# Optimization experiments

Hardware: AMD Instinct MI355X
Metric: run time of the kernel (lower is better)

## Reference

```python
import jax, jax.numpy as jnp
import numpy as np

EPS_MEAN = 1e-10


def setup_inputs() -> dict:
    key = jax.random.key(0)
    ks = jax.random.split(key, 16)
    B, N, F, D = 2, 512, 128, 3
    s = lambda fan_in: 1.0 / np.sqrt(fan_in)
    return {
        "h": jax.random.normal(ks[0], (B, N, F), jnp.float32),
        "coord": jax.random.normal(ks[1], (B, N, D), jnp.float32),
        "mask": jnp.ones((B, N), jnp.float32),
        "edge_w1": jax.random.normal(ks[2], (2 * F + 1, F), jnp.float32) * s(2 * F + 1),
        "edge_b1": jnp.zeros((F,), jnp.float32),
        "edge_w2": jax.random.normal(ks[3], (F, F), jnp.float32) * s(F),
        "edge_b2": jnp.zeros((F,), jnp.float32),
        "node_w1": jax.random.normal(ks[4], (2 * F, F), jnp.float32) * s(2 * F),
        "node_b1": jnp.zeros((F,), jnp.float32),
        "node_w2": jax.random.normal(ks[5], (F, F), jnp.float32) * s(F),
        "node_b2": jnp.zeros((F,), jnp.float32),
        "coord_w1": jax.random.normal(ks[6], (F, F), jnp.float32) * s(F),
        "coord_b1": jnp.zeros((F,), jnp.float32),
        # xavier_uniform with gain=0.001 -> tiny weights
        "coord_w2": jax.random.normal(ks[7], (F, 1), jnp.float32) * 0.001 * s(F),
    }


def reference(h, coord, mask, edge_w1, edge_b1, edge_w2, edge_b2,
              node_w1, node_b1, node_w2, node_b2,
              coord_w1, coord_b1, coord_w2):
    silu = jax.nn.silu
    B, N, F = h.shape
    # mask inputs
    h = h * mask[:, :, None]
    coord = coord * mask[:, :, None]
    mask2d = mask[:, :, None] * mask[:, None, :]            # [B,N,N]

    # coord2radial
    coord_diff = coord[:, :, None] - coord[:, None]          # [B,N,N,3]
    radial = jnp.sum(coord_diff ** 2, axis=-1, keepdims=True)  # [B,N,N,1]
    radial = radial * mask2d[..., None]
    coord_diff = coord_diff * mask2d[..., None]

    # edge model: source[b,i,j]=h[b,j], target[b,i,j]=h[b,i]
    source = jnp.broadcast_to(h[:, None, :, :], (B, N, N, F))
    target = jnp.broadcast_to(h[:, :, None, :], (B, N, N, F))
    edge_in = jnp.concatenate([source, target, radial], axis=-1)  # [B,N,N,2F+1]
    m = silu(edge_in @ edge_w1 + edge_b1)
    m = silu(m @ edge_w2 + edge_b2)                          # [B,N,N,F]
    m = m * mask2d[..., None]

    # coord model
    embed = silu(m @ coord_w1 + coord_b1) @ coord_w2         # [B,N,N,1]
    trans = coord_diff * embed * mask2d[..., None]           # [B,N,N,3]
    denom = jnp.sum(mask2d, axis=2, keepdims=True) + EPS_MEAN  # [B,N,1]
    coord_new = coord + jnp.sum(trans, axis=2) / denom
    coord_new = coord_new * mask[:, :, None]

    # node model
    agg = jnp.sum(m, axis=2)                                 # [B,N,F]
    node_in = jnp.concatenate([h, agg], axis=-1) * mask[:, :, None]
    out = silu(node_in @ node_w1 + node_b1) @ node_w2 + node_b2
    h_new = (h + out) * mask[:, :, None]

    return h_new, coord_new
```

## Files before the change

### kernel.cpp

```cpp
#include <hip/hip_runtime.h>


#define B_ 2
#define N_ 512
#define F_ 128
#define TJ 64
#define MSTRIDE 136

#define CM   (-1.44269504088896340736f)
#define INVC (-0.69314718055994530942f)

typedef __attribute__((ext_vector_type(8))) short short8;
typedef __attribute__((ext_vector_type(4))) float floatx4;
typedef __attribute__((ext_vector_type(2))) float floatx2;

#if defined(__has_builtin)
#if __has_builtin(__builtin_amdgcn_exp2f)
#define EXP2F(x) __builtin_amdgcn_exp2f(x)
#endif
#endif
#ifndef EXP2F
#define EXP2F(x) __expf((x) * 0.69314718055994530942f)
#endif

__device__ __forceinline__ float fsilu(float x) {
    float e = __expf(-x);
    return x * __builtin_amdgcn_rcpf(1.0f + e);
}
__device__ __forceinline__ floatx2 mk2(float a, float b) {
    floatx2 r; r.x = a; r.y = b; return r;
}
__device__ __forceinline__ floatx2 silu2s(floatx2 y) {
    floatx2 e;
    e.x = EXP2F(y.x);
    e.y = EXP2F(y.y);
    floatx2 d = e + 1.0f;
    floatx2 r;
    r.x = __uint_as_float(0x7EF311C3u - __float_as_uint(d.x));
    r.y = __uint_as_float(0x7EF311C3u - __float_as_uint(d.y));
    r = r * (2.0f - d * r);
    r = r * (2.0f - d * r);
    return y * r;
}
__device__ __forceinline__ unsigned cvtpk(float lo, float hi) {
    unsigned r;
    asm("v_cvt_pk_bf16_f32 %0, %1, %2" : "=v"(r) : "v"(lo), "v"(hi));
    return r;
}
__device__ __forceinline__ unsigned pack2(float a, float b) {
    return __builtin_amdgcn_perm(__float_as_uint(b) + 0x8000u,
                                 __float_as_uint(a) + 0x8000u, 0x07060302u);
}

__global__ __launch_bounds__(256) void egcl_prep(
        const float* __restrict__ h, const float* __restrict__ mask,
        const float* __restrict__ ew1, const float* __restrict__ ew2,
        const float* __restrict__ cw1,
        float* __restrict__ Hs, float* __restrict__ Ht,
        unsigned short* __restrict__ W2P, unsigned short* __restrict__ WcP,
        float* __restrict__ msum) {
    __shared__ float sh[8][F_];
    const int blk = blockIdx.x, tid = threadIdx.x;
    if (blk < 128) {
        const int r0 = blk * 8;
        const int col = tid & 127, half = tid >> 7;
#pragma unroll
        for (int rr = 0; rr < 4; ++rr) {
            int row = rr * 2 + half;
            sh[row][col] = h[(r0 + row) * F_ + col] * mask[r0 + row];
        }
        __syncthreads();
        const float* W = ew1 + half * F_ * F_ + col;
        float acc[8] = {0.f, 0.f, 0.f, 0.f, 0.f, 0.f, 0.f, 0.f};
#pragma unroll 8
        for (int k = 0; k < F_; ++k) {
            float w = W[k * F_];
#pragma unroll
            for (int r = 0; r < 8; ++r) acc[r] += sh[r][k] * w;
        }
        float* dst = half ? Ht : Hs;
#pragma unroll
        for (int r = 0; r < 8; ++r) dst[(r0 + r) * F_ + col] = acc[r] * CM;
    } else if (blk < 144) {
        const int wsel = (blk - 128) >> 3;
        const int mt = (blk - 128) & 7;
        const float* src = wsel ? cw1 : ew2;
        unsigned short* dst = wsel ? WcP : W2P;
        const int ln = tid & 63, kk = tid >> 6;
        const int qq = ln >> 4, ll = ln & 15;
#pragma unroll
        for (int rep = 0; rep < 2; ++rep) {
            const int krow = kk * 32 + qq * 8 + rep * 4;
            float f0 = src[(krow + 0) * F_ + mt * 16 + ll];
            float f1 = src[(krow + 1) * F_ + mt * 16 + ll];
            float f2 = src[(krow + 2) * F_ + mt * 16 + ll];
            float f3 = src[(krow + 3) * F_ + mt * 16 + ll];
            uint2 u = make_uint2(pack2(f0, f1), pack2(f2, f3));
            *(uint2*)(dst + ((mt * 4 + kk) * 64 + ln) * 8 + rep * 4) = u;
        }
    } else {
        const int bb = blk - 144;
        float v = mask[bb * N_ + tid] + mask[bb * N_ + 256 + tid];
        v += __shfl_xor(v, 1);  v += __shfl_xor(v, 2);
        v += __shfl_xor(v, 4);  v += __shfl_xor(v, 8);
        v += __shfl_xor(v, 16); v += __shfl_xor(v, 32);
        const int wave = tid >> 6, lane = tid & 63;
        if (lane == 0) sh[0][wave] = v;
        __syncthreads();
        if (tid == 0) msum[bb] = sh[0][0] + sh[0][1] + sh[0][2] + sh[0][3];
    }
}

#define L_M1   0
#define L_M    17408
#define L_HB   34816
#define L_W1R  35328
#define L_EMBP 35840
#define L_HIN  36864
#define L_RAD  37376
#define L_F2   37632
#define L_TOTAL 37888
#define L_AGG  0
#define L_AGGT 512
#define L_TL   1024
#define L_NP   1536
#define L_CSW  2560

__global__ __launch_bounds__(256, 2) void egcl_main(
        const float* __restrict__ h, const float* __restrict__ coord,
        const float* __restrict__ mask,
        const float* __restrict__ eb1, const float* __restrict__ eb2,
        const float* __restrict__ cb1, const float* __restrict__ cw2,
        const float* __restrict__ nw1, const float* __restrict__ nb1,
        const float* __restrict__ nw2, const float* __restrict__ nb2,
        const float* __restrict__ ew1,
        const float* __restrict__ Hs, const float* __restrict__ Ht,
        const unsigned short* __restrict__ W2P,
        const unsigned short* __restrict__ WcP,
        const float* __restrict__ msum,
        float* __restrict__ out_h, float* __restrict__ out_coord) {
    extern __shared__ char smem[];
    unsigned short* m1s = (unsigned short*)(smem + L_M1);
    unsigned short* ms  = (unsigned short*)(smem + L_M);
    float* HB    = (float*)(smem + L_HB);
    float* W1R   = (float*)(smem + L_W1R);
    float* embp  = (float*)(smem + L_EMBP);
    float* hin   = (float*)(smem + L_HIN);
    float* radl  = (float*)(smem + L_RAD);
    float* f2l   = (float*)(smem + L_F2);
    float* aggs  = (float*)(smem + L_AGG);
    float* aggt  = (float*)(smem + L_AGGT);
    float* tl    = (float*)(smem + L_TL);
    float* np    = (float*)(smem + L_NP);
    float* csw   = (float*)(smem + L_CSW);

    const int tid  = threadIdx.x;
    const int wave = tid >> 6, lane = tid & 63;
    const int q = lane >> 4, l15 = lane & 15;
    const int wg = wave;
    const int bi = blockIdx.x;
    const int b  = bi >> 9;
    const float mask_i = mask[bi];

    short8 w2f[2][4], wcf[2][4];
#pragma unroll
    for (int s = 0; s < 2; ++s)
#pragma unroll
        for (int kk = 0; kk < 4; ++kk) {
            w2f[s][kk] = *(const short8*)(W2P + (((2 * wg + s) * 4 + kk) * 64 + lane) * 8);
            wcf[s][kk] = *(const short8*)(WcP + (((2 * wg + s) * 4 + kk) * 64 + lane) * 8);
        }
    floatx4 e2b[2], c1b[2];
    floatx2 w2c2[4];
#pragma unroll
    for (int s = 0; s < 2; ++s) {
        e2b[s] = (*(const floatx4*)(eb2 + wg * 32 + s * 16 + q * 4)) * CM;
        c1b[s] = (*(const floatx4*)(cb1 + wg * 32 + s * 16 + q * 4)) * CM;
    }
    {
        floatx4 w0 = *(const floatx4*)(cw2 + wg * 32 + 0 * 16 + q * 4);
        floatx4 w1 = *(const floatx4*)(cw2 + wg * 32 + 1 * 16 + q * 4);
        w2c2[0] = mk2(w0[0], w0[1]) * INVC;
        w2c2[1] = mk2(w0[2], w0[3]) * INVC;
        w2c2[2] = mk2(w1[0], w1[1]) * INVC;
        w2c2[3] = mk2(w1[2], w1[3]) * INVC;
    }

    if (tid < F_) {
        HB[tid]  = Ht[bi * F_ + tid] + CM * eb1[tid];
        W1R[tid] = CM * ew1[2 * F_ * F_ + tid];
        hin[tid] = h[bi * F_ + tid] * mask_i;
    }
    const float cmi0 = coord[bi * 3 + 0] * mask_i;
    const float cmi1 = coord[bi * 3 + 1] * mask_i;
    const float cmi2 = coord[bi * 3 + 2] * mask_i;
    if (tid < TJ) {
        int jg = b * N_ + tid;
        float mj = mask[jg];
        float c0 = coord[jg * 3 + 0] * mj;
        float c1 = coord[jg * 3 + 1] * mj;
        float c2 = coord[jg * 3 + 2] * mj;
        float d0 = cmi0 - c0, d1 = cmi1 - c1, d2 = cmi2 - c2;
        float ff = mask_i * mj;
        radl[tid] = (d0 * d0 + d1 * d1 + d2 * d2) * ff;
        f2l[tid]  = ff;
    }
    __syncthreads();

    const int kseg = tid & 15, jq = tid >> 4;
    floatx2 hbk2[4], w1k2[4];
    {
        const floatx4* hp = (const floatx4*)(HB + kseg * 8);
        const floatx4* wp = (const floatx4*)(W1R + kseg * 8);
        floatx4 a = hp[0], bb2 = hp[1], cc = wp[0], dd = wp[1];
        hbk2[0] = mk2(a[0], a[1]);   hbk2[1] = mk2(a[2], a[3]);
        hbk2[2] = mk2(bb2[0], bb2[1]); hbk2[3] = mk2(bb2[2], bb2[3]);
        w1k2[0] = mk2(cc[0], cc[1]); w1k2[1] = mk2(cc[2], cc[3]);
        w1k2[2] = mk2(dd[0], dd[1]); w1k2[3] = mk2(dd[2], dd[3]);
    }
    floatx2 ag[4];
    ag[0] = mk2(0.f, 0.f); ag[1] = mk2(0.f, 0.f);
    ag[2] = mk2(0.f, 0.f); ag[3] = mk2(0.f, 0.f);
    float cs0 = 0.f, cs1 = 0.f, cs2 = 0.f;

    for (int p = 0; p < N_ / TJ; ++p) {
#pragma unroll
        for (int r = 0; r < 4; ++r) {
            int row = jq * 4 + r;
            int jg = b * N_ + p * TJ + row;
            float radm = radl[row];
            floatx2 rr = mk2(radm, radm);
            const floatx4* hsp = (const floatx4*)(Hs + jg * F_ + kseg * 8);
            floatx4 h0 = hsp[0], h1 = hsp[1];
            floatx2 y0 = mk2(h0[0], h0[1]) + hbk2[0] + rr * w1k2[0];
            floatx2 y1 = mk2(h0[2], h0[3]) + hbk2[1] + rr * w1k2[1];
            floatx2 y2 = mk2(h1[0], h1[1]) + hbk2[2] + rr * w1k2[2];
            floatx2 y3 = mk2(h1[2], h1[3]) + hbk2[3] + rr * w1k2[3];
            floatx2 x0 = silu2s(y0), x1 = silu2s(y1);
            floatx2 x2 = silu2s(y2), x3 = silu2s(y3);
            union { short8 s8; unsigned u[4]; } pu;
            pu.u[0] = cvtpk(x0.x, x0.y); pu.u[1] = cvtpk(x1.x, x1.y);
            pu.u[2] = cvtpk(x2.x, x2.y); pu.u[3] = cvtpk(x3.x, x3.y);
            *(short8*)(m1s + row * MSTRIDE + kseg * 8) = pu.s8;
        }
        __syncthreads();
#pragma unroll
        for (int jt = 0; jt < 4; ++jt) {
            const int jrow = jt * 16 + l15;
            const unsigned short* m1r = m1s + jrow * MSTRIDE;
            floatx4 a0 = e2b[0], a1 = e2b[1];
#pragma unroll
            for (int kk = 0; kk < 4; ++kk) {
                short8 bf = *(const short8*)(m1r + kk * 32 + q * 8);
                a0 = __builtin_amdgcn_mfma_f32_16x16x32_bf16(w2f[0][kk], bf, a0, 0, 0, 0);
                a1 = __builtin_amdgcn_mfma_f32_16x16x32_bf16(w2f[1][kk], bf, a1, 0, 0, 0);
            }
            const float f2 = f2l[jrow];
            floatx2 f22 = mk2(f2, f2);
            floatx2 p0 = silu2s(mk2(a0[0], a0[1])) * f22;
            floatx2 p1 = silu2s(mk2(a0[2], a0[3])) * f22;
            floatx2 p2 = silu2s(mk2(a1[0], a1[1])) * f22;
            floatx2 p3 = silu2s(mk2(a1[2], a1[3])) * f22;
            ag[0] += p0; ag[1] += p1; ag[2] += p2; ag[3] += p3;
            unsigned short* mr = ms + jrow * MSTRIDE + wg * 32 + q * 4;
            *(uint2*)(mr)      = make_uint2(cvtpk(p0.x, p0.y), cvtpk(p1.x, p1.y));
            *(uint2*)(mr + 16) = make_uint2(cvtpk(p2.x, p2.y), cvtpk(p3.x, p3.y));
        }
        __syncthreads();
#pragma unroll
        for (int jt = 0; jt < 4; ++jt) {
            const int jrow = jt * 16 + l15;
            const unsigned short* mr = ms + jrow * MSTRIDE;
            floatx4 a0 = c1b[0], a1 = c1b[1];
#pragma unroll
            for (int kk = 0; kk < 4; ++kk) {
                short8 bf = *(const short8*)(mr + kk * 32 + q * 8);
                a0 = __builtin_amdgcn_mfma_f32_16x16x32_bf16(wcf[0][kk], bf, a0, 0, 0, 0);
                a1 = __builtin_amdgcn_mfma_f32_16x16x32_bf16(wcf[1][kk], bf, a1, 0, 0, 0);
            }
            floatx2 esv = mk2(0.f, 0.f);
            esv += silu2s(mk2(a0[0], a0[1])) * w2c2[0];
            esv += silu2s(mk2(a0[2], a0[3])) * w2c2[1];
            esv += silu2s(mk2(a1[0], a1[1])) * w2c2[2];
            esv += silu2s(mk2(a1[2], a1[3])) * w2c2[3];
            float es = esv.x + esv.y;
            es += __shfl_xor(es, 16);
            es += __shfl_xor(es, 32);
            if (q == 0) embp[wg * 64 + jrow] = es;
        }
        if (p < N_ / TJ - 1 && wave == 1) {
            int jg = b * N_ + (p + 1) * TJ + lane;
            float mj = mask[jg];
            float c0 = coord[jg * 3 + 0] * mj;
            float c1 = coord[jg * 3 + 1] * mj;
            float c2 = coord[jg * 3 + 2] * mj;
            float d0 = cmi0 - c0, d1 = cmi1 - c1, d2 = cmi2 - c2;
            float ff = mask_i * mj;
            radl[lane] = (d0 * d0 + d1 * d1 + d2 * d2) * ff;
            f2l[lane]  = ff;
        }
        __syncthreads();
        if (tid < TJ) {
            float e = embp[tid] + embp[64 + tid] + embp[128 + tid] + embp[192 + tid];
            int jg = b * N_ + p * TJ + tid;
            float mj = mask[jg];
            float c0 = coord[jg * 3 + 0] * mj;
            float c1 = coord[jg * 3 + 1] * mj;
            float c2 = coord[jg * 3 + 2] * mj;
            float f2 = mask_i * mj;
            float w = e * f2 * f2;
            cs0 += (cmi0 - c0) * w;
            cs1 += (cmi1 - c1) * w;
            cs2 += (cmi2 - c2) * w;
        }
    }

    float agf[8] = {ag[0].x, ag[0].y, ag[1].x, ag[1].y,
                    ag[2].x, ag[2].y, ag[3].x, ag[3].y};
#pragma unroll
    for (int rg = 0; rg < 8; ++rg) {
        float v = agf[rg];
        v += __shfl_xor(v, 1); v += __shfl_xor(v, 2);
        v += __shfl_xor(v, 4); v += __shfl_xor(v, 8);
        agf[rg] = v;
    }
    if (l15 == 0) {
        floatx4 o0 = {agf[0], agf[1], agf[2], agf[3]};
        floatx4 o1 = {agf[4], agf[5], agf[6], agf[7]};
        *(floatx4*)(aggs + wg * 32 + q * 4)      = o0;
        *(floatx4*)(aggs + wg * 32 + 16 + q * 4) = o1;
    }
    if (wave == 0) {
        cs0 += __shfl_xor(cs0, 1); cs0 += __shfl_xor(cs0, 2);
        cs0 += __shfl_xor(cs0, 4); cs0 += __shfl_xor(cs0, 8);
        cs0 += __shfl_xor(cs0, 16); cs0 += __shfl_xor(cs0, 32);
        cs1 += __shfl_xor(cs1, 1); cs1 += __shfl_xor(cs1, 2);
        cs1 += __shfl_xor(cs1, 4); cs1 += __shfl_xor(cs1, 8);
        cs1 += __shfl_xor(cs1, 16); cs1 += __shfl_xor(cs1, 32);
        cs2 += __shfl_xor(cs2, 1); cs2 += __shfl_xor(cs2, 2);
        cs2 += __shfl_xor(cs2, 4); cs2 += __shfl_xor(cs2, 8);
        cs2 += __shfl_xor(cs2, 16); cs2 += __shfl_xor(cs2, 32);
        if (lane == 0) {
            csw[0] = cs0; csw[1] = cs1; csw[2] = cs2;
        }
    }
    __syncthreads();
    if (tid < F_) aggt[tid] = aggs[tid] * (mask_i * INVC);
    __syncthreads();
    {
        int half = tid >> 7, col = tid & 127;
        const float* W = nw1 + half * 128 * F_ + col;
        float s = 0.f;
        if (half == 0) {
#pragma unroll 8
            for (int k = 0; k < F_; ++k) s += hin[k] * W[k * F_];
            s *= mask_i;
        } else {
#pragma unroll 8
            for (int k = 0; k < F_; ++k) s += aggt[k] * W[k * F_];
        }
        np[tid] = s;
    }
    __syncthreads();
    if (tid < F_) tl[tid] = fsilu(np[tid] + np[128 + tid] + nb1[tid]);
    __syncthreads();
    if (tid < F_) {
        float s = nb2[tid];
#pragma unroll 8
        for (int k = 0; k < F_; ++k) s += tl[k] * nw2[k * F_ + tid];
        out_h[bi * F_ + tid] = (hin[tid] + s) * mask_i;
    } else if (tid < F_ + 3) {
        int d = tid - F_;
        float denom = mask_i * msum[b] + 1e-10f;
        float cm = (d == 0) ? cmi0 : ((d == 1) ? cmi1 : cmi2);
        out_coord[bi * 3 + d] = (cm + csw[d] * __builtin_amdgcn_rcpf(denom)) * mask_i;
    }
}

extern "C" void kernel_launch(void* const* d_in, const int* in_sizes, int n_in,
                              void* d_out, int out_size, void* d_ws, size_t ws_size,
                              hipStream_t stream) {
    const float* h     = (const float*)d_in[0];
    const float* coord = (const float*)d_in[1];
    const float* mask  = (const float*)d_in[2];
    const float* ew1   = (const float*)d_in[3];
    const float* eb1   = (const float*)d_in[4];
    const float* ew2   = (const float*)d_in[5];
    const float* eb2   = (const float*)d_in[6];
    const float* nw1   = (const float*)d_in[7];
    const float* nb1   = (const float*)d_in[8];
    const float* nw2   = (const float*)d_in[9];
    const float* nb2   = (const float*)d_in[10];
    const float* cw1   = (const float*)d_in[11];
    const float* cb1   = (const float*)d_in[12];
    const float* cw2   = (const float*)d_in[13];

    float* Hs = (float*)d_ws;
    float* Ht = Hs + B_ * N_ * F_;
    unsigned short* W2P = (unsigned short*)(Ht + B_ * N_ * F_);
    unsigned short* WcP = W2P + F_ * F_;
    float* msum = (float*)(WcP + F_ * F_);

    float* out_h = (float*)d_out;
    float* out_coord = out_h + B_ * N_ * F_;

    egcl_prep<<<146, 256, 0, stream>>>(h, mask, ew1, ew2, cw1,
                                       Hs, Ht, W2P, WcP, msum);
    egcl_main<<<B_ * N_, 256, L_TOTAL, stream>>>(
        h, coord, mask, eb1, eb2, cb1, cw2, nw1, nb1, nw2, nb2, ew1,
        Hs, Ht, W2P, WcP, msum, out_h, out_coord);
}
```

Measured before the change: 177.5 us.

## Restructure edge loop: per-wave row ownership with register layer-1 fragments and LDS weights

The block grows to 512 threads, and each wave owns 32 neighbour rows per pass, with the j-tile enlarged to 256. The first edge layer is computed straight into MFMA B-fragments in registers instead of being staged through shared memory. The per-iteration block barriers and cross-wave embedding reduction are removed: edge and coord weights are copied once per block into a large LDS region, and each wave reduces its own coordinate partials. In exchange, LDS use rises to about 138KB per block, which limits occupancy. Every block also re-copies 64KB of packed weights from global memory, and weight fragments are re-read from LDS on every MFMA step instead of sitting in registers.

```diff
diff --git a/kernel.cpp b/kernel.cpp
--- a/kernel.cpp
+++ b/kernel.cpp
@@ -4,7 +4,7 @@
 #define B_ 2
 #define N_ 512
 #define F_ 128
-#define TJ 64
+#define TJ 256
 #define MSTRIDE 136
 
 #define CM   (-1.44269504088896340736f)
@@ -111,22 +111,23 @@
     }
 }
 
-#define L_M1   0
-#define L_M    17408
-#define L_HB   34816
-#define L_W1R  35328
-#define L_EMBP 35840
-#define L_HIN  36864
-#define L_RAD  37376
-#define L_F2   37632
-#define L_TOTAL 37888
-#define L_AGG  0
-#define L_AGGT 512
-#define L_TL   1024
-#define L_NP   1536
-#define L_CSW  2560
-
-__global__ __launch_bounds__(256, 2) void egcl_main(
+#define L_W2   0
+#define L_WC   32768
+#define L_MS   65536
+#define L_HB   135168
+#define L_W1R  135680
+#define L_EB2  136192
+#define L_CB1  136704
+#define L_CW2  137216
+#define L_HIN  137728
+#define L_TOTAL 138240
+#define L_AGGP (L_MS + 0)
+#define L_CSP  (L_MS + 4096)
+#define L_NP   (L_MS + 4224)
+#define L_TL   (L_MS + 6272)
+#define L_AGGT (L_MS + 6784)
+
+__global__ __launch_bounds__(512, 2) void egcl_main(
         const float* __restrict__ h, const float* __restrict__ coord,
         const float* __restrict__ mask,
         const float* __restrict__ eb1, const float* __restrict__ eb2,
@@ -140,229 +141,229 @@
         const float* __restrict__ msum,
         float* __restrict__ out_h, float* __restrict__ out_coord) {
     extern __shared__ char smem[];
-    unsigned short* m1s = (unsigned short*)(smem + L_M1);
-    unsigned short* ms  = (unsigned short*)(smem + L_M);
+    unsigned short* W2L = (unsigned short*)(smem + L_W2);
+    unsigned short* WcL = (unsigned short*)(smem + L_WC);
+    unsigned short* ms  = (unsigned short*)(smem + L_MS);
     float* HB    = (float*)(smem + L_HB);
     float* W1R   = (float*)(smem + L_W1R);
-    float* embp  = (float*)(smem + L_EMBP);
+    float* EB2s  = (float*)(smem + L_EB2);
+    float* CB1s  = (float*)(smem + L_CB1);
+    float* CW2s  = (float*)(smem + L_CW2);
     float* hin   = (float*)(smem + L_HIN);
-    float* radl  = (float*)(smem + L_RAD);
-    float* f2l   = (float*)(smem + L_F2);
-    float* aggs  = (float*)(smem + L_AGG);
+    float* aggp  = (float*)(smem + L_AGGP);
+    float* csp   = (float*)(smem + L_CSP);
+    float* np    = (float*)(smem + L_NP);
+    float* tl    = (float*)(smem + L_TL);
     float* aggt  = (float*)(smem + L_AGGT);
-    float* tl    = (float*)(smem + L_TL);
-    float* np    = (float*)(smem + L_NP);
-    float* csw   = (float*)(smem + L_CSW);
 
     const int tid  = threadIdx.x;
     const int wave = tid >> 6, lane = tid & 63;
     const int q = lane >> 4, l15 = lane & 15;
-    const int wg = wave;
     const int bi = blockIdx.x;
     const int b  = bi >> 9;
     const float mask_i = mask[bi];
 
-    short8 w2f[2][4], wcf[2][4];
-#pragma unroll
-    for (int s = 0; s < 2; ++s)
-#pragma unroll
-        for (int kk = 0; kk < 4; ++kk) {
-            w2f[s][kk] = *(const short8*)(W2P + (((2 * wg + s) * 4 + kk) * 64 + lane) * 8);
-            wcf[s][kk] = *(const short8*)(WcP + (((2 * wg + s) * 4 + kk) * 64 + lane) * 8);
-        }
-    floatx4 e2b[2], c1b[2];
-    floatx2 w2c2[4];
-#pragma unroll
-    for (int s = 0; s < 2; ++s) {
-        e2b[s] = (*(const floatx4*)(eb2 + wg * 32 + s * 16 + q * 4)) * CM;
-        c1b[s] = (*(const floatx4*)(cb1 + wg * 32 + s * 16 + q * 4)) * CM;
-    }
     {
-        floatx4 w0 = *(const floatx4*)(cw2 + wg * 32 + 0 * 16 + q * 4);
-        floatx4 w1 = *(const floatx4*)(cw2 + wg * 32 + 1 * 16 + q * 4);
-        w2c2[0] = mk2(w0[0], w0[1]) * INVC;
-        w2c2[1] = mk2(w0[2], w0[3]) * INVC;
-        w2c2[2] = mk2(w1[0], w1[1]) * INVC;
-        w2c2[3] = mk2(w1[2], w1[3]) * INVC;
-    }
-
+        const uint4* s2 = (const uint4*)W2P;
+        const uint4* sc = (const uint4*)WcP;
+        uint4* d2 = (uint4*)(smem + L_W2);
+        uint4* dc = (uint4*)(smem + L_WC);
+#pragma unroll
+        for (int t = 0; t < 4; ++t) {
+            d2[tid + t * 512] = s2[tid + t * 512];
+            dc[tid + t * 512] = sc[tid + t * 512];
+        }
+    }
     if (tid < F_) {
-        HB[tid]  = Ht[bi * F_ + tid] + CM * eb1[tid];
-        W1R[tid] = CM * ew1[2 * F_ * F_ + tid];
-        hin[tid] = h[bi * F_ + tid] * mask_i;
+        HB[tid]   = Ht[bi * F_ + tid] + CM * eb1[tid];
+        W1R[tid]  = CM * ew1[2 * F_ * F_ + tid];
+        EB2s[tid] = CM * eb2[tid];
+        CB1s[tid] = CM * cb1[tid];
+        CW2s[tid] = INVC * cw2[tid];
+        hin[tid]  = h[bi * F_ + tid] * mask_i;
     }
     const float cmi0 = coord[bi * 3 + 0] * mask_i;
     const float cmi1 = coord[bi * 3 + 1] * mask_i;
     const float cmi2 = coord[bi * 3 + 2] * mask_i;
-    if (tid < TJ) {
-        int jg = b * N_ + tid;
-        float mj = mask[jg];
-        float c0 = coord[jg * 3 + 0] * mj;
-        float c1 = coord[jg * 3 + 1] * mj;
-        float c2 = coord[jg * 3 + 2] * mj;
-        float d0 = cmi0 - c0, d1 = cmi1 - c1, d2 = cmi2 - c2;
-        float ff = mask_i * mj;
-        radl[tid] = (d0 * d0 + d1 * d1 + d2 * d2) * ff;
-        f2l[tid]  = ff;
-    }
-    __syncthreads();
-
-    const int kseg = tid & 15, jq = tid >> 4;
-    floatx2 hbk2[4], w1k2[4];
+    __syncthreads();
+
+    const int j0 = wave * 32 + l15;
+    const int j1 = j0 + 16;
+    unsigned short* msr0 = ms + j0 * MSTRIDE;
+    unsigned short* msr1 = ms + j1 * MSTRIDE;
+
+    floatx2 ag2[16];
+#pragma unroll
+    for (int t = 0; t < 16; ++t) ag2[t] = mk2(0.f, 0.f);
+    float cs0 = 0.f, cs1 = 0.f, cs2 = 0.f;
+
+    for (int p = 0; p < N_ / TJ; ++p) {
+        const int jg0 = b * N_ + p * TJ + j0;
+        const int jg1 = jg0 + 16;
+        const float mj0 = mask[jg0], mj1 = mask[jg1];
+        const float c00 = coord[jg0 * 3 + 0] * mj0;
+        const float c01 = coord[jg0 * 3 + 1] * mj0;
+        const float c02 = coord[jg0 * 3 + 2] * mj0;
+        const float c10 = coord[jg1 * 3 + 0] * mj1;
+        const float c11 = coord[jg1 * 3 + 1] * mj1;
+        const float c12 = coord[jg1 * 3 + 2] * mj1;
+        const float d00 = cmi0 - c00, d01 = cmi1 - c01, d02 = cmi2 - c02;
+        const float d10 = cmi0 - c10, d11 = cmi1 - c11, d12 = cmi2 - c12;
+        const float f2_0 = mask_i * mj0, f2_1 = mask_i * mj1;
+        const float rad0 = (d00 * d00 + d01 * d01 + d02 * d02) * f2_0;
+        const float rad1 = (d10 * d10 + d11 * d11 + d12 * d12) * f2_1;
+        const floatx2 rr0 = mk2(rad0, rad0), rr1 = mk2(rad1, rad1);
+        const floatx2 f220 = mk2(f2_0, f2_0), f221 = mk2(f2_1, f2_1);
+
+        short8 bfr0[4], bfr1[4];
+#pragma unroll
+        for (int kk = 0; kk < 4; ++kk) {
+            const int ko = kk * 32 + q * 8;
+            floatx4 hb0 = *(const floatx4*)(HB + ko);
+            floatx4 hb1 = *(const floatx4*)(HB + ko + 4);
+            floatx4 w10 = *(const floatx4*)(W1R + ko);
+            floatx4 w11 = *(const floatx4*)(W1R + ko + 4);
+            {
+                floatx4 hsA = *(const floatx4*)(Hs + jg0 * F_ + ko);
+                floatx4 hsB = *(const floatx4*)(Hs + jg0 * F_ + ko + 4);
+                floatx2 y0 = mk2(hsA[0], hsA[1]) + mk2(hb0[0], hb0[1]) + rr0 * mk2(w10[0], w10[1]);
+                floatx2 y1 = mk2(hsA[2], hsA[3]) + mk2(hb0[2], hb0[3]) + rr0 * mk2(w10[2], w10[3]);
+                floatx2 y2 = mk2(hsB[0], hsB[1]) + mk2(hb1[0], hb1[1]) + rr0 * mk2(w11[0], w11[1]);
+                floatx2 y3 = mk2(hsB[2], hsB[3]) + mk2(hb1[2], hb1[3]) + rr0 * mk2(w11[2], w11[3]);
+                floatx2 x0 = silu2s(y0), x1 = silu2s(y1);
+                floatx2 x2 = silu2s(y2), x3 = silu2s(y3);
+                union { short8 s8; unsigned u[4]; } pu;
+                pu.u[0] = cvtpk(x0.x, x0.y); pu.u[1] = cvtpk(x1.x, x1.y);
+                pu.u[2] = cvtpk(x2.x, x2.y); pu.u[3] = cvtpk(x3.x, x3.y);
+                bfr0[kk] = pu.s8;
+            }
+            {
+                floatx4 hsA = *(const floatx4*)(Hs + jg1 * F_ + ko);
+                floatx4 hsB = *(const floatx4*)(Hs + jg1 * F_ + ko + 4);
+                floatx2 y0 = mk2(hsA[0], hsA[1]) + mk2(hb0[0], hb0[1]) + rr1 * mk2(w10[0], w10[1]);
+                floatx2 y1 = mk2(hsA[2], hsA[3]) + mk2(hb0[2], hb0[3]) + rr1 * mk2(w10[2], w10[3]);
+                floatx2 y2 = mk2(hsB[0], hsB[1]) + mk2(hb1[0], hb1[1]) + rr1 * mk2(w11[0], w11[1]);
+                floatx2 y3 = mk2(hsB[2], hsB[3]) + mk2(hb1[2], hb1[3]) + rr1 * mk2(w11[2], w11[3]);
+                floatx2 x0 = silu2s(y0), x1 = silu2s(y1);
+                floatx2 x2 = silu2s(y2), x3 = silu2s(y3);
+                union { short8 s8; unsigned u[4]; } pu;
+                pu.u[0] = cvtpk(x0.x, x0.y); pu.u[1] = cvtpk(x1.x, x1.y);
+                pu.u[2] = cvtpk(x2.x, x2.y); pu.u[3] = cvtpk(x3.x, x3.y);
+                bfr1[kk] = pu.s8;
+            }
+        }
+
+#pragma unroll
+        for (int s = 0; s < 8; ++s) {
+            floatx4 bias = *(const floatx4*)(EB2s + s * 16 + q * 4);
+            floatx4 a0 = bias, a1 = bias;
+#pragma unroll
+            for (int kk = 0; kk < 4; ++kk) {
+                short8 wf = *(const short8*)(W2L + ((s * 4 + kk) * 64 + lane) * 8);
+                a0 = __builtin_amdgcn_mfma_f32_16x16x32_bf16(wf, bfr0[kk], a0, 0, 0, 0);
+                a1 = __builtin_amdgcn_mfma_f32_16x16x32_bf16(wf, bfr1[kk], a1, 0, 0, 0);
+            }
+            floatx2 p00 = silu2s(mk2(a0[0], a0[1])) * f220;
+            floatx2 p01 = silu2s(mk2(a0[2], a0[3])) * f220;
+            floatx2 p10 = silu2s(mk2(a1[0], a1[1])) * f221;
+            floatx2 p11 = silu2s(mk2(a1[2], a1[3])) * f221;
+            ag2[2 * s]     += p00 + p10;
+            ag2[2 * s + 1] += p01 + p11;
+            *(uint2*)(msr0 + s * 16 + q * 4) =
+                make_uint2(cvtpk(p00.x, p00.y), cvtpk(p01.x, p01.y));
+            *(uint2*)(msr1 + s * 16 + q * 4) =
+                make_uint2(cvtpk(p10.x, p10.y), cvtpk(p11.x, p11.y));
+        }
+
+        short8 mfr0[4], mfr1[4];
+#pragma unroll
+        for (int kk = 0; kk < 4; ++kk) {
+            mfr0[kk] = *(const short8*)(msr0 + kk * 32 + q * 8);
+            mfr1[kk] = *(const short8*)(msr1 + kk * 32 + q * 8);
+        }
+        floatx2 esv0 = mk2(0.f, 0.f), esv1 = mk2(0.f, 0.f);
+#pragma unroll
+        for (int s = 0; s < 8; ++s) {
+            floatx4 cb = *(const floatx4*)(CB1s + s * 16 + q * 4);
+            floatx4 a0 = cb, a1 = cb;
+#pragma unroll
+            for (int kk = 0; kk < 4; ++kk) {
+                short8 wf = *(const short8*)(WcL + ((s * 4 + kk) * 64 + lane) * 8);
+                a0 = __builtin_amdgcn_mfma_f32_16x16x32_bf16(wf, mfr0[kk], a0, 0, 0, 0);
+                a1 = __builtin_amdgcn_mfma_f32_16x16x32_bf16(wf, mfr1[kk], a1, 0, 0, 0);
+            }
+            floatx4 wv = *(const floatx4*)(CW2s + s * 16 + q * 4);
+            esv0 += silu2s(mk2(a0[0], a0[1])) * mk2(wv[0], wv[1]);
+            esv0 += silu2s(mk2(a0[2], a0[3])) * mk2(wv[2], wv[3]);
+            esv1 += silu2s(mk2(a1[0], a1[1])) * mk2(wv[0], wv[1]);
+            esv1 += silu2s(mk2(a1[2], a1[3])) * mk2(wv[2], wv[3]);
+        }
+        float es0 = esv0.x + esv0.y;
+        float es1 = esv1.x + esv1.y;
+        es0 += __shfl_xor(es0, 16); es0 += __shfl_xor(es0, 32);
+        es1 += __shfl_xor(es1, 16); es1 += __shfl_xor(es1, 32);
+        if (q == 0) {
+            float w0 = es0 * f2_0 * f2_0;
+            float w1 = es1 * f2_1 * f2_1;
+            cs0 += d00 * w0 + d10 * w1;
+            cs1 += d01 * w0 + d11 * w1;
+            cs2 += d02 * w0 + d12 * w1;
+        }
+    }
+
+#pragma unroll
+    for (int t = 0; t < 16; ++t) {
+        float vx = ag2[t].x, vy = ag2[t].y;
+        vx += __shfl_xor(vx, 1); vx += __shfl_xor(vx, 2);
+        vx += __shfl_xor(vx, 4); vx += __shfl_xor(vx, 8);
+        vy += __shfl_xor(vy, 1); vy += __shfl_xor(vy, 2);
+        vy += __shfl_xor(vy, 4); vy += __shfl_xor(vy, 8);
+        ag2[t] = mk2(vx, vy);
+    }
+    cs0 += __shfl_xor(cs0, 1); cs0 += __shfl_xor(cs0, 2);
+    cs0 += __shfl_xor(cs0, 4); cs0 += __shfl_xor(cs0, 8);
+    cs1 += __shfl_xor(cs1, 1); cs1 += __shfl_xor(cs1, 2);
+    cs1 += __shfl_xor(cs1, 4); cs1 += __shfl_xor(cs1, 8);
+    cs2 += __shfl_xor(cs2, 1); cs2 += __shfl_xor(cs2, 2);
+    cs2 += __shfl_xor(cs2, 4); cs2 += __shfl_xor(cs2, 8);
+
+    __syncthreads();
+    if (l15 == 0) {
+#pragma unroll
+        for (int s = 0; s < 8; ++s) {
+            floatx4 o = {ag2[2 * s].x, ag2[2 * s].y,
+                         ag2[2 * s + 1].x, ag2[2 * s + 1].y};
+            *(floatx4*)(aggp + wave * F_ + s * 16 + q * 4) = o;
+        }
+    }
+    if (lane == 0) {
+        csp[wave * 3 + 0] = cs0;
+        csp[wave * 3 + 1] = cs1;
+        csp[wave * 3 + 2] = cs2;
+    }
+    __syncthreads();
+    if (tid < F_) {
+        float s = 0.f;
+#pragma unroll
+        for (int w = 0; w < 8; ++w) s += aggp[w * F_ + tid];
+        aggt[tid] = s * (mask_i * INVC);
+    }
+    __syncthreads();
     {
-        const floatx4* hp = (const floatx4*)(HB + kseg * 8);
-        const floatx4* wp = (const floatx4*)(W1R + kseg * 8);
-        floatx4 a = hp[0], bb2 = hp[1], cc = wp[0], dd = wp[1];
-        hbk2[0] = mk2(a[0], a[1]);   hbk2[1] = mk2(a[2], a[3]);
-        hbk2[2] = mk2(bb2[0], bb2[1]); hbk2[3] = mk2(bb2[2], bb2[3]);
-        w1k2[0] = mk2(cc[0], cc[1]); w1k2[1] = mk2(cc[2], cc[3]);
-        w1k2[2] = mk2(dd[0], dd[1]); w1k2[3] = mk2(dd[2], dd[3]);
-    }
-    floatx2 ag[4];
-    ag[0] = mk2(0.f, 0.f); ag[1] = mk2(0.f, 0.f);
-    ag[2] = mk2(0.f, 0.f); ag[3] = mk2(0.f, 0.f);
-    float cs0 = 0.f, cs1 = 0.f, cs2 = 0.f;
-
-    for (int p = 0; p < N_ / TJ; ++p) {
-#pragma unroll
-        for (int r = 0; r < 4; ++r) {
-            int row = jq * 4 + r;
-            int jg = b * N_ + p * TJ + row;
-            float radm = radl[row];
-            floatx2 rr = mk2(radm, radm);
-            const floatx4* hsp = (const floatx4*)(Hs + jg * F_ + kseg * 8);
-            floatx4 h0 = hsp[0], h1 = hsp[1];
-            floatx2 y0 = mk2(h0[0], h0[1]) + hbk2[0] + rr * w1k2[0];
-            floatx2 y1 = mk2(h0[2], h0[3]) + hbk2[1] + rr * w1k2[1];
-            floatx2 y2 = mk2(h1[0], h1[1]) + hbk2[2] + rr * w1k2[2];
-            floatx2 y3 = mk2(h1[2], h1[3]) + hbk2[3] + rr * w1k2[3];
-            floatx2 x0 = silu2s(y0), x1 = silu2s(y1);
-            floatx2 x2 = silu2s(y2), x3 = silu2s(y3);
-            union { short8 s8; unsigned u[4]; } pu;
-            pu.u[0] = cvtpk(x0.x, x0.y); pu.u[1] = cvtpk(x1.x, x1.y);
-            pu.u[2] = cvtpk(x2.x, x2.y); pu.u[3] = cvtpk(x3.x, x3.y);
-            *(short8*)(m1s + row * MSTRIDE + kseg * 8) = pu.s8;
-        }
-        __syncthreads();
-#pragma unroll
-        for (int jt = 0; jt < 4; ++jt) {
-            const int jrow = jt * 16 + l15;
-            const unsigned short* m1r = m1s + jrow * MSTRIDE;
-            floatx4 a0 = e2b[0], a1 = e2b[1];
-#pragma unroll
-            for (int kk = 0; kk < 4; ++kk) {
-                short8 bf = *(const short8*)(m1r + kk * 32 + q * 8);
-                a0 = __builtin_amdgcn_mfma_f32_16x16x32_bf16(w2f[0][kk], bf, a0, 0, 0, 0);
-                a1 = __builtin_amdgcn_mfma_f32_16x16x32_bf16(w2f[1][kk], bf, a1, 0, 0, 0);
-            }
-            const float f2 = f2l[jrow];
-            floatx2 f22 = mk2(f2, f2);
-            floatx2 p0 = silu2s(mk2(a0[0], a0[1])) * f22;
-            floatx2 p1 = silu2s(mk2(a0[2], a0[3])) * f22;
-            floatx2 p2 = silu2s(mk2(a1[0], a1[1])) * f22;
-            floatx2 p3 = silu2s(mk2(a1[2], a1[3])) * f22;
-            ag[0] += p0; ag[1] += p1; ag[2] += p2; ag[3] += p3;
-            unsigned short* mr = ms + jrow * MSTRIDE + wg * 32 + q * 4;
-            *(uint2*)(mr)      = make_uint2(cvtpk(p0.x, p0.y), cvtpk(p1.x, p1.y));
-            *(uint2*)(mr + 16) = make_uint2(cvtpk(p2.x, p2.y), cvtpk(p3.x, p3.y));
-        }
-        __syncthreads();
-#pragma unroll
-        for (int jt = 0; jt < 4; ++jt) {
-            const int jrow = jt * 16 + l15;
-            const unsigned short* mr = ms + jrow * MSTRIDE;
-            floatx4 a0 = c1b[0], a1 = c1b[1];
-#pragma unroll
-            for (int kk = 0; kk < 4; ++kk) {
-                short8 bf = *(const short8*)(mr + kk * 32 + q * 8);
-                a0 = __builtin_amdgcn_mfma_f32_16x16x32_bf16(wcf[0][kk], bf, a0, 0, 0, 0);
-                a1 = __builtin_amdgcn_mfma_f32_16x16x32_bf16(wcf[1][kk], bf, a1, 0, 0, 0);
-            }
-            floatx2 esv = mk2(0.f, 0.f);
-            esv += silu2s(mk2(a0[0], a0[1])) * w2c2[0];
-            esv += silu2s(mk2(a0[2], a0[3])) * w2c2[1];
-            esv += silu2s(mk2(a1[0], a1[1])) * w2c2[2];
-            esv += silu2s(mk2(a1[2], a1[3])) * w2c2[3];
-            float es = esv.x + esv.y;
-            es += __shfl_xor(es, 16);
-            es += __shfl_xor(es, 32);
-            if (q == 0) embp[wg * 64 + jrow] = es;
-        }
-        if (p < N_ / TJ - 1 && wave == 1) {
-            int jg = b * N_ + (p + 1) * TJ + lane;
-            float mj = mask[jg];
-            float c0 = coord[jg * 3 + 0] * mj;
-            float c1 = coord[jg * 3 + 1] * mj;
-            float c2 = coord[jg * 3 + 2] * mj;
-            float d0 = cmi0 - c0, d1 = cmi1 - c1, d2 = cmi2 - c2;
-            float ff = mask_i * mj;
-            radl[lane] = (d0 * d0 + d1 * d1 + d2 * d2) * ff;
-            f2l[lane]  = ff;
-        }
-        __syncthreads();
-        if (tid < TJ) {
-            float e = embp[tid] + embp[64 + tid] + embp[128 + tid] + embp[192 + tid];
-            int jg = b * N_ + p * TJ + tid;
-            float mj = mask[jg];
-            float c0 = coord[jg * 3 + 0] * mj;
-            float c1 = coord[jg * 3 + 1] * mj;
-            float c2 = coord[jg * 3 + 2] * mj;
-            float f2 = mask_i * mj;
-            float w = e * f2 * f2;
-            cs0 += (cmi0 - c0) * w;
-            cs1 += (cmi1 - c1) * w;
-            cs2 += (cmi2 - c2) * w;
-        }
-    }
-
-    float agf[8] = {ag[0].x, ag[0].y, ag[1].x, ag[1].y,
-                    ag[2].x, ag[2].y, ag[3].x, ag[3].y};
-#pragma unroll
-    for (int rg = 0; rg < 8; ++rg) {
-        float v = agf[rg];
-        v += __shfl_xor(v, 1); v += __shfl_xor(v, 2);
-        v += __shfl_xor(v, 4); v += __shfl_xor(v, 8);
-        agf[rg] = v;
-    }
-    if (l15 == 0) {
-        floatx4 o0 = {agf[0], agf[1], agf[2], agf[3]};
-        floatx4 o1 = {agf[4], agf[5], agf[6], agf[7]};
-        *(floatx4*)(aggs + wg * 32 + q * 4)      = o0;
-        *(floatx4*)(aggs + wg * 32 + 16 + q * 4) = o1;
-    }
-    if (wave == 0) {
-        cs0 += __shfl_xor(cs0, 1); cs0 += __shfl_xor(cs0, 2);
-        cs0 += __shfl_xor(cs0, 4); cs0 += __shfl_xor(cs0, 8);
-        cs0 += __shfl_xor(cs0, 16); cs0 += __shfl_xor(cs0, 32);
-        cs1 += __shfl_xor(cs1, 1); cs1 += __shfl_xor(cs1, 2);
-        cs1 += __shfl_xor(cs1, 4); cs1 += __shfl_xor(cs1, 8);
-        cs1 += __shfl_xor(cs1, 16); cs1 += __shfl_xor(cs1, 32);
-        cs2 += __shfl_xor(cs2, 1); cs2 += __shfl_xor(cs2, 2);
-        cs2 += __shfl_xor(cs2, 4); cs2 += __shfl_xor(cs2, 8);
-        cs2 += __shfl_xor(cs2, 16); cs2 += __shfl_xor(cs2, 32);
-        if (lane == 0) {
-            csw[0] = cs0; csw[1] = cs1; csw[2] = cs2;
-        }
-    }
-    __syncthreads();
-    if (tid < F_) aggt[tid] = aggs[tid] * (mask_i * INVC);
-    __syncthreads();
-    {
-        int half = tid >> 7, col = tid & 127;
-        const float* W = nw1 + half * 128 * F_ + col;
+        const int col = tid & 127, q2 = tid >> 7;
+        const int half = q2 & 1, kh = q2 >> 1;
+        const float* W = nw1 + (half * 128 + kh * 64) * F_ + col;
+        const float* src = half ? (aggt + kh * 64) : (hin + kh * 64);
         float s = 0.f;
-        if (half == 0) {
 #pragma unroll 8
-            for (int k = 0; k < F_; ++k) s += hin[k] * W[k * F_];
-            s *= mask_i;
-        } else {
-#pragma unroll 8
-            for (int k = 0; k < F_; ++k) s += aggt[k] * W[k * F_];
-        }
+        for (int k = 0; k < 64; ++k) s += src[k] * W[k * F_];
+        if (half == 0) s *= mask_i;
         np[tid] = s;
     }
     __syncthreads();
-    if (tid < F_) tl[tid] = fsilu(np[tid] + np[128 + tid] + nb1[tid]);
+    if (tid < F_)
+        tl[tid] = fsilu(np[tid] + np[128 + tid] + np[256 + tid] +
+                        np[384 + tid] + nb1[tid]);
     __syncthreads();
     if (tid < F_) {
         float s = nb2[tid];
@@ -373,7 +374,10 @@
         int d = tid - F_;
         float denom = mask_i * msum[b] + 1e-10f;
         float cm = (d == 0) ? cmi0 : ((d == 1) ? cmi1 : cmi2);
-        out_coord[bi * 3 + d] = (cm + csw[d] * __builtin_amdgcn_rcpf(denom)) * mask_i;
+        float cst = 0.f;
+#pragma unroll
+        for (int w = 0; w < 8; ++w) cst += csp[w * 3 + d];
+        out_coord[bi * 3 + d] = (cm + cst * __builtin_amdgcn_rcpf(denom)) * mask_i;
     }
 }
 
@@ -404,9 +408,17 @@
     float* out_h = (float*)d_out;
     float* out_coord = out_h + B_ * N_ * F_;
 
+    static int attr_done = 0;
+    if (!attr_done) {
+        (void)hipFuncSetAttribute((const void*)egcl_main,
+                                  hipFuncAttributeMaxDynamicSharedMemorySize,
+                                  L_TOTAL);
+        attr_done = 1;
+    }
+
     egcl_prep<<<146, 256, 0, stream>>>(h, mask, ew1, ew2, cw1,
                                        Hs, Ht, W2P, WcP, msum);
-    egcl_main<<<B_ * N_, 256, L_TOTAL, stream>>>(
+    egcl_main<<<B_ * N_, 512, L_TOTAL, stream>>>(
         h, coord, mask, eb1, eb2, cb1, cw2, nw1, nb1, nw2, nb2, ew1,
         Hs, Ht, W2P, WcP, msum, out_h, out_coord);
 }
```

After: 193.6 us. 9.1% more time.
